# Optimization experiments

Measured on AMD Instinct MI355X. Metric: run time of the kernel, lower is better.

## Reference

```python
import math
import itertools
import jax, jax.numpy as jnp
import numpy as np

QUALITY = 95
FACTOR = (200.0 - 2.0 * QUALITY) / 100.0  # quality>=50 branch -> 0.1

# ---- constant tables (match original torch Parameters) ----
_Y = np.array([
    [16, 11, 10, 16, 24, 40, 51, 61],
    [12, 12, 14, 19, 26, 58, 60, 55],
    [14, 13, 16, 24, 40, 57, 69, 56],
    [14, 17, 22, 29, 51, 87, 80, 62],
    [18, 22, 37, 56, 68, 109, 103, 77],
    [24, 35, 55, 64, 81, 104, 113, 92],
    [49, 64, 78, 87, 103, 121, 120, 101],
    [72, 92, 95, 98, 112, 100, 103, 99]], dtype=np.float32)
Y_TABLE = jnp.asarray(_Y.T)
_C = np.full((8, 8), 99.0, dtype=np.float32)
_C[:4, :4] = np.array([[17, 18, 24, 47], [18, 21, 26, 66],
                       [24, 26, 56, 99], [47, 66, 99, 99]], dtype=np.float32).T
C_TABLE = jnp.asarray(_C)

RGB2YCBCR = jnp.asarray(np.array([
    [0.299, 0.587, 0.114],
    [-0.168736, -0.331264, 0.5],
    [0.5, -0.418688, -0.081312]], dtype=np.float32))
YCBCR2RGB = jnp.asarray(np.array([
    [1.0, 0.0, 1.402],
    [1.0, -0.344136, -0.714136],
    [1.0, 1.772, 0.0]], dtype=np.float32))

_cosmat = np.cos((2 * np.arange(8)[:, None] + 1) * np.arange(8)[None, :] * np.pi / 16).astype(np.float32)  # [x,u]
DCT_T = jnp.asarray(np.einsum('xu,yv->xyuv', _cosmat, _cosmat))   # tensor[x,y,u,v]
IDCT_T = jnp.asarray(np.einsum('ux,vy->xyuv', _cosmat, _cosmat))  # cos((2u+1)x..)cos((2v+1)y..)
_alpha = np.array([1.0 / np.sqrt(2)] + [1.0] * 7, dtype=np.float32)
ALPHA = jnp.asarray(np.outer(_alpha, _alpha))
DCT_SCALE = ALPHA * 0.25


def diff_round(x):
    s = jnp.zeros_like(x)
    for n in range(1, 10):
        s = s + ((-1.0) ** (n + 1) / n) * jnp.sin(2.0 * math.pi * n * x)
    return x - s / math.pi


def _avgpool2(x):  # [B,H,W] -> [B,H/2,W/2]
    b, h, w = x.shape
    return x.reshape(b, h // 2, 2, w // 2, 2).mean(axis=(2, 4))


def _block_split(x):  # [B,H,W] -> [B,N,8,8]
    b, h, w = x.shape
    return x.reshape(b, h // 8, 8, w // 8, 8).transpose(0, 1, 3, 2, 4).reshape(b, -1, 8, 8)


def _block_merge(p, h, w):  # [B,N,8,8] -> [B,h,w]
    b = p.shape[0]
    return p.reshape(b, h // 8, w // 8, 8, 8).transpose(0, 1, 3, 2, 4).reshape(b, h, w)


def _compress_component(comp, table):
    blocks = _block_split(comp) - 128.0
    dct = DCT_SCALE * jnp.einsum('bnxy,xyuv->bnuv', blocks, DCT_T)
    return diff_round(dct / (table * FACTOR))


def _decompress_component(q, table, h, w):
    d = q * (table * FACTOR)
    idct = 0.25 * jnp.einsum('bnxy,xyuv->bnuv', d * ALPHA, IDCT_T) + 128.0
    return _block_merge(idct, h, w)


def _diffjpeg(x):
    b, c, h, w = x.shape
    img = x * 255.0
    # RGB -> YCbCr (pixel @ RGB2YCBCR.T) + shift
    ycbcr = jnp.einsum('bchw,oc->bhwo', img, RGB2YCBCR) + jnp.array([0.0, 128.0, 128.0], dtype=x.dtype)
    y = ycbcr[..., 0]
    cb = _avgpool2(ycbcr[..., 1])
    cr = _avgpool2(ycbcr[..., 2])
    # compress
    yq = _compress_component(y, Y_TABLE)
    cbq = _compress_component(cb, C_TABLE)
    crq = _compress_component(cr, C_TABLE)
    # decompress
    y2 = _decompress_component(yq, Y_TABLE, h, w)
    cb2 = _decompress_component(cbq, C_TABLE, h // 2, w // 2)
    cr2 = _decompress_component(crq, C_TABLE, h // 2, w // 2)
    cb_up = jnp.repeat(jnp.repeat(cb2, 2, axis=1), 2, axis=2)
    cr_up = jnp.repeat(jnp.repeat(cr2, 2, axis=1), 2, axis=2)
    ycc = jnp.stack([y2, cb_up, cr_up], axis=3)  # [B,H,W,3]
    rgb = jnp.einsum('bhwc,oc->bhwo', ycc + jnp.array([0.0, -128.0, -128.0], dtype=x.dtype), YCBCR2RGB)
    rgb = rgb.transpose(0, 3, 1, 2)  # [B,3,H,W]
    rgb = jnp.clip(rgb, 0.0, 255.0)
    return rgb / 255.0


def setup_inputs() -> dict:
    key = jax.random.key(0)
    x = jax.random.uniform(key, (16, 3, 512, 512), dtype=jnp.float32)
    return {"x": x}


def reference(x):
    return _diffjpeg(x)
```

## Files before the change

kernel.cpp:

```cpp
#include <hip/hip_runtime.h>
#include <hip/hip_bf16.h>


__device__ constexpr float YTAB8[8][8] = {
    {16, 12, 14, 14, 18, 24, 49, 72},
    {11, 12, 13, 17, 22, 35, 64, 92},
    {10, 14, 16, 22, 37, 55, 78, 95},
    {16, 19, 24, 29, 56, 64, 87, 98},
    {24, 26, 40, 51, 68, 81, 103, 112},
    {40, 58, 57, 87, 109, 104, 121, 100},
    {51, 60, 69, 80, 103, 113, 120, 103},
    {61, 55, 56, 62, 77, 92, 101, 99}};

__device__ constexpr float CTAB8[8][8] = {
    {17, 18, 24, 47, 99, 99, 99, 99},
    {18, 21, 26, 66, 99, 99, 99, 99},
    {24, 26, 56, 99, 99, 99, 99, 99},
    {47, 66, 99, 99, 99, 99, 99, 99},
    {99, 99, 99, 99, 99, 99, 99, 99},
    {99, 99, 99, 99, 99, 99, 99, 99},
    {99, 99, 99, 99, 99, 99, 99, 99},
    {99, 99, 99, 99, 99, 99, 99, 99}};

#define C1f 0.9807852804032304f
#define C2f 0.9238795325112867f
#define C3f 0.8314696123025452f
#define C4f 0.7071067811865476f
#define C5f 0.5555702330196022f
#define C6f 0.3826834323650898f
#define C7f 0.1950903220161283f

__device__ __forceinline__ void dct8(float y[8]) {
    float e0=y[0]+y[7], e1=y[1]+y[6], e2=y[2]+y[5], e3=y[3]+y[4];
    float o0=y[0]-y[7], o1=y[1]-y[6], o2=y[2]-y[5], o3=y[3]-y[4];
    float t0=e0+e3, t1=e1+e2, d0=e0-e3, d1=e1-e2;
    y[0]=t0+t1; y[4]=(t0-t1)*C4f;
    y[2]=d0*C2f+d1*C6f; y[6]=d0*C6f-d1*C2f;
    y[1]=o0*C1f+o1*C3f+o2*C5f+o3*C7f;
    y[3]=o0*C3f-o1*C7f-o2*C1f-o3*C5f;
    y[5]=o0*C5f-o1*C1f+o2*C7f+o3*C3f;
    y[7]=o0*C7f-o1*C5f+o2*C3f-o3*C1f;
}

__device__ __forceinline__ void idct8(float y[8]) {
    float a=y[4]*C4f, p=y[0]+a, m=y[0]-a;
    float q=y[2]*C2f+y[6]*C6f, w=y[2]*C6f-y[6]*C2f;
    float E0=p+q, E1=m+w, E2=m-w, E3=p-q;
    float O0=y[1]*C1f+y[3]*C3f+y[5]*C5f+y[7]*C7f;
    float O1=y[1]*C3f-y[3]*C7f-y[5]*C1f-y[7]*C5f;
    float O2=y[1]*C5f-y[3]*C1f+y[5]*C7f+y[7]*C3f;
    float O3=y[1]*C7f-y[3]*C5f+y[5]*C3f-y[7]*C1f;
    y[0]=E0+O0; y[7]=E0-O0; y[1]=E1+O1; y[6]=E1-O1;
    y[2]=E2+O2; y[5]=E2-O2; y[3]=E3+O3; y[4]=E3-O3;
}

__device__ __forceinline__ void transpose8(float y[8]) {
    const int lane = threadIdx.x & 63;
#pragma unroll
    for (int s = 1; s <= 4; s <<= 1) {
        const bool upper = (lane & (s << 3)) != 0;
#pragma unroll
        for (int j = 0; j < 8; ++j) {
            if ((j & s) == 0) {
                float a = y[j], b2 = y[j | s];
                float t = upper ? a : b2;
                t = __shfl_xor(t, s << 3, 64);
                if (upper) y[j] = t; else y[j | s] = t;
            }
        }
    }
}

__device__ __forceinline__ float diff_round_f(float x) {
    float f = x - rintf(x);
    float th = 6.283185307179586f * f;
    float s1, c1v;
    __sincosf(th, &s1, &c1v);
    float twoc = 2.0f * c1v;
    float sp = 0.0f, sc = s1, acc = 0.0f;
    const float coef[9] = {1.0f, -0.5f, 1.0f/3.0f, -0.25f, 0.2f,
                           -1.0f/6.0f, 1.0f/7.0f, -0.125f, 1.0f/9.0f};
#pragma unroll
    for (int n = 0; n < 9; ++n) {
        acc += coef[n] * sc;
        float sn = twoc * sc - sp;
        sp = sc; sc = sn;
    }
    return x - acc * 0.3183098861837907f;
}

__global__ __launch_bounds__(384, 6) void diffjpeg_kernel(
        const float* __restrict__ x, float* __restrict__ out) {
    __shared__ float QS[2][128];
    __shared__ float PL[3][8][65];
    __shared__ float CL[2][8][65];

    const int tid = threadIdx.x;
    const int lane = tid & 63;
    const int r = lane >> 3;
    const int b = lane & 7;

    if (tid < 128) {
        int type = tid >> 6;
        int k = tid & 63, u = k >> 3, v = k & 7;
        float t = (type ? CTAB8[u][v] : YTAB8[u][v]) * 0.1f;
        float aa = 0.25f * ((u == 0) ? C4f : 1.0f) * ((v == 0) ? C4f : 1.0f);
        QS[type][2 * k]     = aa / t;
        QS[type][2 * k + 1] = aa * t;
    }

    const int img = blockIdx.y;
    const int sy = (blockIdx.x >> 2) * 16;
    const int sx = (blockIdx.x & 3) * 128;
    const size_t plane = (size_t)512 * 512;
    const float* src = x + (size_t)img * 3 * plane;
    float* dst = out + (size_t)img * 3 * plane;

    float y[8];
    const int w = tid >> 6;
    const int brow = w >> 1;
    const int bcol = (w & 1) * 8 + b;

    if (tid < 256) {
        const int py = sy + brow * 8 + r;
        const int px = sx + bcol * 8;
        const float* p = src + (size_t)py * 512 + px;
        float4 R0 = *(const float4*)(p);
        float4 R1 = *(const float4*)(p + 4);
        float4 G0 = *(const float4*)(p + plane);
        float4 G1 = *(const float4*)(p + plane + 4);
        float4 B0 = *(const float4*)(p + 2 * plane);
        float4 B1 = *(const float4*)(p + 2 * plane + 4);
        y[0] = 76.245f * R0.x + 149.685f * G0.x + 29.07f * B0.x - 128.0f;
        y[1] = 76.245f * R0.y + 149.685f * G0.y + 29.07f * B0.y - 128.0f;
        y[2] = 76.245f * R0.z + 149.685f * G0.z + 29.07f * B0.z - 128.0f;
        y[3] = 76.245f * R0.w + 149.685f * G0.w + 29.07f * B0.w - 128.0f;
        y[4] = 76.245f * R1.x + 149.685f * G1.x + 29.07f * B1.x - 128.0f;
        y[5] = 76.245f * R1.y + 149.685f * G1.y + 29.07f * B1.y - 128.0f;
        y[6] = 76.245f * R1.z + 149.685f * G1.z + 29.07f * B1.z - 128.0f;
        y[7] = 76.245f * R1.w + 149.685f * G1.w + 29.07f * B1.w - 128.0f;
        float rs0 = R0.x + R0.y, rs1 = R0.z + R0.w, rs2 = R1.x + R1.y, rs3 = R1.z + R1.w;
        float gs0 = G0.x + G0.y, gs1 = G0.z + G0.w, gs2 = G1.x + G1.y, gs3 = G1.z + G1.w;
        float bs0 = B0.x + B0.y, bs1 = B0.z + B0.w, bs2 = B1.x + B1.y, bs3 = B1.z + B1.w;
        rs0 += __shfl_xor(rs0, 8, 64); rs1 += __shfl_xor(rs1, 8, 64);
        rs2 += __shfl_xor(rs2, 8, 64); rs3 += __shfl_xor(rs3, 8, 64);
        gs0 += __shfl_xor(gs0, 8, 64); gs1 += __shfl_xor(gs1, 8, 64);
        gs2 += __shfl_xor(gs2, 8, 64); gs3 += __shfl_xor(gs3, 8, 64);
        bs0 += __shfl_xor(bs0, 8, 64); bs1 += __shfl_xor(bs1, 8, 64);
        bs2 += __shfl_xor(bs2, 8, 64); bs3 += __shfl_xor(bs3, 8, 64);
        if (!(r & 1)) {
            const int prow = brow * 4 + (r >> 1);
            const int pc = bcol * 4;
            PL[0][prow][pc] = rs0; PL[0][prow][pc+1] = rs1;
            PL[0][prow][pc+2] = rs2; PL[0][prow][pc+3] = rs3;
            PL[1][prow][pc] = gs0; PL[1][prow][pc+1] = gs1;
            PL[1][prow][pc+2] = gs2; PL[1][prow][pc+3] = gs3;
            PL[2][prow][pc] = bs0; PL[2][prow][pc+1] = bs1;
            PL[2][prow][pc+2] = bs2; PL[2][prow][pc+3] = bs3;
        }
    }
    __syncthreads();

    if (tid < 256) {
        dct8(y); transpose8(y); dct8(y);
        const float* qs = QS[0];
#pragma unroll
        for (int j = 0; j < 8; ++j) {
            float s1v = qs[2 * (j * 8 + r)];
            float s2v = qs[2 * (j * 8 + r) + 1];
            y[j] = diff_round_f(y[j] * s1v) * s2v;
        }
        idct8(y); transpose8(y); idct8(y);
    } else {
        const int ch = (tid >= 320);
        const float kr = ch ?  31.875f   : -10.75692f;
        const float kg = ch ? -26.69136f : -21.11808f;
        const float kb = ch ?  -5.18364f :  31.875f;
        float c[8];
#pragma unroll
        for (int j = 0; j < 8; ++j)
            c[j] = kr * PL[0][r][b * 8 + j] + kg * PL[1][r][b * 8 + j]
                 + kb * PL[2][r][b * 8 + j];
        dct8(c); transpose8(c); dct8(c);
        const float* qs = QS[1];
#pragma unroll
        for (int j = 0; j < 8; ++j) {
            float s1v = qs[2 * (j * 8 + r)];
            float s2v = qs[2 * (j * 8 + r) + 1];
            c[j] = diff_round_f(c[j] * s1v) * s2v;
        }
        idct8(c); transpose8(c); idct8(c);
#pragma unroll
        for (int j = 0; j < 8; ++j)
            CL[ch][r][b * 8 + j] = c[j];
    }
    __syncthreads();

    if (tid < 256) {
        const int prow = brow * 4 + (r >> 1);
        const int pc = bcol * 4;
        float cbv[4], crv[4];
#pragma unroll
        for (int jj = 0; jj < 4; ++jj) {
            cbv[jj] = CL[0][prow][pc + jj];
            crv[jj] = CL[1][prow][pc + jj];
        }
        float oR[8], oG[8], oB[8];
#pragma unroll
        for (int j = 0; j < 8; ++j) {
            float cb = cbv[j >> 1], cr = crv[j >> 1];
            float yv = y[j] + 128.0f;
            float R = yv + 1.402f * cr;
            float G = yv - 0.344136f * cb - 0.714136f * cr;
            float B = yv + 1.772f * cb;
            oR[j] = fminf(fmaxf(R, 0.0f), 255.0f) * (1.0f / 255.0f);
            oG[j] = fminf(fmaxf(G, 0.0f), 255.0f) * (1.0f / 255.0f);
            oB[j] = fminf(fmaxf(B, 0.0f), 255.0f) * (1.0f / 255.0f);
        }
        const int py = sy + brow * 8 + r;
        const int px = sx + bcol * 8;
        float* p = dst + (size_t)py * 512 + px;
        *(float4*)(p)                 = make_float4(oR[0], oR[1], oR[2], oR[3]);
        *(float4*)(p + 4)             = make_float4(oR[4], oR[5], oR[6], oR[7]);
        *(float4*)(p + plane)         = make_float4(oG[0], oG[1], oG[2], oG[3]);
        *(float4*)(p + plane + 4)     = make_float4(oG[4], oG[5], oG[6], oG[7]);
        *(float4*)(p + 2 * plane)     = make_float4(oB[0], oB[1], oB[2], oB[3]);
        *(float4*)(p + 2 * plane + 4) = make_float4(oB[4], oB[5], oB[6], oB[7]);
    }
}

extern "C" void kernel_launch(void* const* d_in, const int* in_sizes, int n_in,
                              void* d_out, int out_size, void* d_ws, size_t ws_size,
                              hipStream_t stream) {
    const float* x = (const float*)d_in[0];
    float* out = (float*)d_out;
    dim3 grid(128, 16);
    dim3 block(384);
    diffjpeg_kernel<<<grid, block, 0, stream>>>(x, out);
}
```

Before: 27.36 us.

## Process 32-row tiles with 256 threads, balancing luma and chroma work per wave

Each block now covers a 32x128 tile with 256 threads. Every thread handles two luma blocks and one chroma block, so the separate chroma waves that sat idle during the luma phase are gone. Chroma conversion is folded in before the pair-sum shuffle, which shrinks the shared staging to two chroma planes. diff_round now uses hardware fract/sin/cos builtins that take revolutions directly, dropping the rint and the 2*pi multiply. The trade-offs are more registers per thread and half as many blocks.

```diff
diff --git a/kernel.cpp b/kernel.cpp
--- a/kernel.cpp
+++ b/kernel.cpp
@@ -1,5 +1,4 @@
 #include <hip/hip_runtime.h>
-#include <hip/hip_bf16.h>
 
 
 __device__ constexpr float YTAB8[8][8] = {
@@ -72,12 +71,11 @@
 }
 
 __device__ __forceinline__ float diff_round_f(float x) {
-    float f = x - rintf(x);
-    float th = 6.283185307179586f * f;
-    float s1, c1v;
-    __sincosf(th, &s1, &c1v);
+    float f = __builtin_amdgcn_fractf(x);
+    float sc = __builtin_amdgcn_sinf(f);
+    float c1v = __builtin_amdgcn_cosf(f);
     float twoc = 2.0f * c1v;
-    float sp = 0.0f, sc = s1, acc = 0.0f;
+    float sp = 0.0f, acc = 0.0f;
     const float coef[9] = {1.0f, -0.5f, 1.0f/3.0f, -0.25f, 0.2f,
                            -1.0f/6.0f, 1.0f/7.0f, -0.125f, 1.0f/9.0f};
 #pragma unroll
@@ -89,16 +87,28 @@
     return x - acc * 0.3183098861837907f;
 }
 
-__global__ __launch_bounds__(384, 6) void diffjpeg_kernel(
+__device__ __forceinline__ void jpeg_block(float y[8], const float* qs, int r) {
+    dct8(y); transpose8(y); dct8(y);
+#pragma unroll
+    for (int j = 0; j < 8; ++j) {
+        float s1v = qs[2 * (j * 8 + r)];
+        float s2v = qs[2 * (j * 8 + r) + 1];
+        y[j] = diff_round_f(y[j] * s1v) * s2v;
+    }
+    idct8(y); transpose8(y); idct8(y);
+}
+
+__global__ __launch_bounds__(256, 4) void diffjpeg_kernel(
         const float* __restrict__ x, float* __restrict__ out) {
     __shared__ float QS[2][128];
-    __shared__ float PL[3][8][65];
-    __shared__ float CL[2][8][65];
+    __shared__ float PL[2][16][65];
+    __shared__ float CL[2][16][65];
 
     const int tid = threadIdx.x;
     const int lane = tid & 63;
     const int r = lane >> 3;
     const int b = lane & 7;
+    const int w = tid >> 6;
 
     if (tid < 128) {
         int type = tid >> 6;
@@ -110,95 +120,118 @@
     }
 
     const int img = blockIdx.y;
-    const int sy = (blockIdx.x >> 2) * 16;
+    const int sy = (blockIdx.x >> 2) * 32;
     const int sx = (blockIdx.x & 3) * 128;
     const size_t plane = (size_t)512 * 512;
     const float* src = x + (size_t)img * 3 * plane;
     float* dst = out + (size_t)img * 3 * plane;
 
-    float y[8];
-    const int w = tid >> 6;
-    const int brow = w >> 1;
-    const int bcol = (w & 1) * 8 + b;
-
-    if (tid < 256) {
-        const int py = sy + brow * 8 + r;
-        const int px = sx + bcol * 8;
-        const float* p = src + (size_t)py * 512 + px;
-        float4 R0 = *(const float4*)(p);
-        float4 R1 = *(const float4*)(p + 4);
-        float4 G0 = *(const float4*)(p + plane);
-        float4 G1 = *(const float4*)(p + plane + 4);
-        float4 B0 = *(const float4*)(p + 2 * plane);
-        float4 B1 = *(const float4*)(p + 2 * plane + 4);
-        y[0] = 76.245f * R0.x + 149.685f * G0.x + 29.07f * B0.x - 128.0f;
-        y[1] = 76.245f * R0.y + 149.685f * G0.y + 29.07f * B0.y - 128.0f;
-        y[2] = 76.245f * R0.z + 149.685f * G0.z + 29.07f * B0.z - 128.0f;
-        y[3] = 76.245f * R0.w + 149.685f * G0.w + 29.07f * B0.w - 128.0f;
-        y[4] = 76.245f * R1.x + 149.685f * G1.x + 29.07f * B1.x - 128.0f;
-        y[5] = 76.245f * R1.y + 149.685f * G1.y + 29.07f * B1.y - 128.0f;
-        y[6] = 76.245f * R1.z + 149.685f * G1.z + 29.07f * B1.z - 128.0f;
-        y[7] = 76.245f * R1.w + 149.685f * G1.w + 29.07f * B1.w - 128.0f;
-        float rs0 = R0.x + R0.y, rs1 = R0.z + R0.w, rs2 = R1.x + R1.y, rs3 = R1.z + R1.w;
-        float gs0 = G0.x + G0.y, gs1 = G0.z + G0.w, gs2 = G1.x + G1.y, gs3 = G1.z + G1.w;
-        float bs0 = B0.x + B0.y, bs1 = B0.z + B0.w, bs2 = B1.x + B1.y, bs3 = B1.z + B1.w;
-        rs0 += __shfl_xor(rs0, 8, 64); rs1 += __shfl_xor(rs1, 8, 64);
-        rs2 += __shfl_xor(rs2, 8, 64); rs3 += __shfl_xor(rs3, 8, 64);
-        gs0 += __shfl_xor(gs0, 8, 64); gs1 += __shfl_xor(gs1, 8, 64);
-        gs2 += __shfl_xor(gs2, 8, 64); gs3 += __shfl_xor(gs3, 8, 64);
-        bs0 += __shfl_xor(bs0, 8, 64); bs1 += __shfl_xor(bs1, 8, 64);
-        bs2 += __shfl_xor(bs2, 8, 64); bs3 += __shfl_xor(bs3, 8, 64);
+    const int browA = w >> 1;
+    const int bcol  = (w & 1) * 8 + b;
+    const int px  = sx + bcol * 8;
+    const int pyA = sy + browA * 8 + r;
+    const int pyB = pyA + 16;
+
+    float yA[8], yB[8];
+    {
+        const float* pa = src + (size_t)pyA * 512 + px;
+        const float* pb = src + (size_t)pyB * 512 + px;
+        float4 RA0 = *(const float4*)(pa);
+        float4 RA1 = *(const float4*)(pa + 4);
+        float4 GA0 = *(const float4*)(pa + plane);
+        float4 GA1 = *(const float4*)(pa + plane + 4);
+        float4 BA0 = *(const float4*)(pa + 2 * plane);
+        float4 BA1 = *(const float4*)(pa + 2 * plane + 4);
+        float4 RB0 = *(const float4*)(pb);
+        float4 RB1 = *(const float4*)(pb + 4);
+        float4 GB0 = *(const float4*)(pb + plane);
+        float4 GB1 = *(const float4*)(pb + plane + 4);
+        float4 BB0 = *(const float4*)(pb + 2 * plane);
+        float4 BB1 = *(const float4*)(pb + 2 * plane + 4);
+
+        yA[0] = 76.245f*RA0.x + 149.685f*GA0.x + 29.07f*BA0.x - 128.0f;
+        yA[1] = 76.245f*RA0.y + 149.685f*GA0.y + 29.07f*BA0.y - 128.0f;
+        yA[2] = 76.245f*RA0.z + 149.685f*GA0.z + 29.07f*BA0.z - 128.0f;
+        yA[3] = 76.245f*RA0.w + 149.685f*GA0.w + 29.07f*BA0.w - 128.0f;
+        yA[4] = 76.245f*RA1.x + 149.685f*GA1.x + 29.07f*BA1.x - 128.0f;
+        yA[5] = 76.245f*RA1.y + 149.685f*GA1.y + 29.07f*BA1.y - 128.0f;
+        yA[6] = 76.245f*RA1.z + 149.685f*GA1.z + 29.07f*BA1.z - 128.0f;
+        yA[7] = 76.245f*RA1.w + 149.685f*GA1.w + 29.07f*BA1.w - 128.0f;
+        yB[0] = 76.245f*RB0.x + 149.685f*GB0.x + 29.07f*BB0.x - 128.0f;
+        yB[1] = 76.245f*RB0.y + 149.685f*GB0.y + 29.07f*BB0.y - 128.0f;
+        yB[2] = 76.245f*RB0.z + 149.685f*GB0.z + 29.07f*BB0.z - 128.0f;
+        yB[3] = 76.245f*RB0.w + 149.685f*GB0.w + 29.07f*BB0.w - 128.0f;
+        yB[4] = 76.245f*RB1.x + 149.685f*GB1.x + 29.07f*BB1.x - 128.0f;
+        yB[5] = 76.245f*RB1.y + 149.685f*GB1.y + 29.07f*BB1.y - 128.0f;
+        yB[6] = 76.245f*RB1.z + 149.685f*GB1.z + 29.07f*BB1.z - 128.0f;
+        yB[7] = 76.245f*RB1.w + 149.685f*GB1.w + 29.07f*BB1.w - 128.0f;
+
+        const float kbr = -10.75692f, kbg = -21.11808f, kbb = 31.875f;
+        const float krr =  31.875f,   krg = -26.69136f, krb = -5.18364f;
+        float cbA[4], crA[4], cbB[4], crB[4];
+        {
+            float rh0=RA0.x+RA0.y, rh1=RA0.z+RA0.w, rh2=RA1.x+RA1.y, rh3=RA1.z+RA1.w;
+            float gh0=GA0.x+GA0.y, gh1=GA0.z+GA0.w, gh2=GA1.x+GA1.y, gh3=GA1.z+GA1.w;
+            float bh0=BA0.x+BA0.y, bh1=BA0.z+BA0.w, bh2=BA1.x+BA1.y, bh3=BA1.z+BA1.w;
+            cbA[0]=kbr*rh0+kbg*gh0+kbb*bh0; cbA[1]=kbr*rh1+kbg*gh1+kbb*bh1;
+            cbA[2]=kbr*rh2+kbg*gh2+kbb*bh2; cbA[3]=kbr*rh3+kbg*gh3+kbb*bh3;
+            crA[0]=krr*rh0+krg*gh0+krb*bh0; crA[1]=krr*rh1+krg*gh1+krb*bh1;
+            crA[2]=krr*rh2+krg*gh2+krb*bh2; crA[3]=krr*rh3+krg*gh3+krb*bh3;
+        }
+        {
+            float rh0=RB0.x+RB0.y, rh1=RB0.z+RB0.w, rh2=RB1.x+RB1.y, rh3=RB1.z+RB1.w;
+            float gh0=GB0.x+GB0.y, gh1=GB0.z+GB0.w, gh2=GB1.x+GB1.y, gh3=GB1.z+GB1.w;
+            float bh0=BB0.x+BB0.y, bh1=BB0.z+BB0.w, bh2=BB1.x+BB1.y, bh3=BB1.z+BB1.w;
+            cbB[0]=kbr*rh0+kbg*gh0+kbb*bh0; cbB[1]=kbr*rh1+kbg*gh1+kbb*bh1;
+            cbB[2]=kbr*rh2+kbg*gh2+kbb*bh2; cbB[3]=kbr*rh3+kbg*gh3+kbb*bh3;
+            crB[0]=krr*rh0+krg*gh0+krb*bh0; crB[1]=krr*rh1+krg*gh1+krb*bh1;
+            crB[2]=krr*rh2+krg*gh2+krb*bh2; crB[3]=krr*rh3+krg*gh3+krb*bh3;
+        }
+#pragma unroll
+        for (int k = 0; k < 4; ++k) {
+            cbA[k] += __shfl_xor(cbA[k], 8, 64);
+            crA[k] += __shfl_xor(crA[k], 8, 64);
+            cbB[k] += __shfl_xor(cbB[k], 8, 64);
+            crB[k] += __shfl_xor(crB[k], 8, 64);
+        }
         if (!(r & 1)) {
-            const int prow = brow * 4 + (r >> 1);
+            const int prowA = browA * 4 + (r >> 1);
+            const int prowB = prowA + 8;
             const int pc = bcol * 4;
-            PL[0][prow][pc] = rs0; PL[0][prow][pc+1] = rs1;
-            PL[0][prow][pc+2] = rs2; PL[0][prow][pc+3] = rs3;
-            PL[1][prow][pc] = gs0; PL[1][prow][pc+1] = gs1;
-            PL[1][prow][pc+2] = gs2; PL[1][prow][pc+3] = gs3;
-            PL[2][prow][pc] = bs0; PL[2][prow][pc+1] = bs1;
-            PL[2][prow][pc+2] = bs2; PL[2][prow][pc+3] = bs3;
+#pragma unroll
+            for (int k = 0; k < 4; ++k) {
+                PL[0][prowA][pc + k] = cbA[k];
+                PL[1][prowA][pc + k] = crA[k];
+                PL[0][prowB][pc + k] = cbB[k];
+                PL[1][prowB][pc + k] = crB[k];
+            }
         }
     }
     __syncthreads();
 
-    if (tid < 256) {
-        dct8(y); transpose8(y); dct8(y);
-        const float* qs = QS[0];
-#pragma unroll
-        for (int j = 0; j < 8; ++j) {
-            float s1v = qs[2 * (j * 8 + r)];
-            float s2v = qs[2 * (j * 8 + r) + 1];
-            y[j] = diff_round_f(y[j] * s1v) * s2v;
-        }
-        idct8(y); transpose8(y); idct8(y);
-    } else {
-        const int ch = (tid >= 320);
-        const float kr = ch ?  31.875f   : -10.75692f;
-        const float kg = ch ? -26.69136f : -21.11808f;
-        const float kb = ch ?  -5.18364f :  31.875f;
+    jpeg_block(yA, QS[0], r);
+    jpeg_block(yB, QS[0], r);
+
+    {
+        const int chw  = w >> 1;
+        const int cblk = (w & 1) * 8 + b;
+        const int crow = (cblk >> 3) * 8 + r;
+        const int ccol = (cblk & 7) * 8;
         float c[8];
 #pragma unroll
-        for (int j = 0; j < 8; ++j)
-            c[j] = kr * PL[0][r][b * 8 + j] + kg * PL[1][r][b * 8 + j]
-                 + kb * PL[2][r][b * 8 + j];
-        dct8(c); transpose8(c); dct8(c);
-        const float* qs = QS[1];
-#pragma unroll
-        for (int j = 0; j < 8; ++j) {
-            float s1v = qs[2 * (j * 8 + r)];
-            float s2v = qs[2 * (j * 8 + r) + 1];
-            c[j] = diff_round_f(c[j] * s1v) * s2v;
-        }
-        idct8(c); transpose8(c); idct8(c);
-#pragma unroll
-        for (int j = 0; j < 8; ++j)
-            CL[ch][r][b * 8 + j] = c[j];
+        for (int j = 0; j < 8; ++j) c[j] = PL[chw][crow][ccol + j];
+        jpeg_block(c, QS[1], r);
+#pragma unroll
+        for (int j = 0; j < 8; ++j) CL[chw][crow][ccol + j] = c[j];
     }
     __syncthreads();
 
-    if (tid < 256) {
-        const int prow = brow * 4 + (r >> 1);
-        const int pc = bcol * 4;
+    const int pc = bcol * 4;
+#pragma unroll
+    for (int blkI = 0; blkI < 2; ++blkI) {
+        const float* yv8 = blkI ? yB : yA;
+        const int prow = browA * 4 + (r >> 1) + blkI * 8;
+        const int py   = blkI ? pyB : pyA;
         float cbv[4], crv[4];
 #pragma unroll
         for (int jj = 0; jj < 4; ++jj) {
@@ -209,7 +242,7 @@
 #pragma unroll
         for (int j = 0; j < 8; ++j) {
             float cb = cbv[j >> 1], cr = crv[j >> 1];
-            float yv = y[j] + 128.0f;
+            float yv = yv8[j] + 128.0f;
             float R = yv + 1.402f * cr;
             float G = yv - 0.344136f * cb - 0.714136f * cr;
             float B = yv + 1.772f * cb;
@@ -217,8 +250,6 @@
             oG[j] = fminf(fmaxf(G, 0.0f), 255.0f) * (1.0f / 255.0f);
             oB[j] = fminf(fmaxf(B, 0.0f), 255.0f) * (1.0f / 255.0f);
         }
-        const int py = sy + brow * 8 + r;
-        const int px = sx + bcol * 8;
         float* p = dst + (size_t)py * 512 + px;
         *(float4*)(p)                 = make_float4(oR[0], oR[1], oR[2], oR[3]);
         *(float4*)(p + 4)             = make_float4(oR[4], oR[5], oR[6], oR[7]);
@@ -234,7 +265,7 @@
                               hipStream_t stream) {
     const float* x = (const float*)d_in[0];
     float* out = (float*)d_out;
-    dim3 grid(128, 16);
-    dim3 block(384);
+    dim3 grid(64, 16);
+    dim3 block(256);
     diffjpeg_kernel<<<grid, block, 0, stream>>>(x, out);
 }
```

Result: faster. 25.72 us (-6.0%).

## Use single-wave blocks with per-block chroma and hardware sin/cos rounding

Applied to the files above, without the earlier changes.

Shrinks each block to one 64-lane wave covering a 16x32 tile. Every wave now handles its own luma blocks plus the chroma blocks, instead of 6-wave blocks where two waves sit idle during luma work. Chroma Cb/Cr are computed before the shuffle reduction, so only two planes go to LDS instead of three. diff_round now uses the hardware fract, sin and cos builtins, which take revolutions directly, in place of rintf plus __sincosf. The risks are redundant chroma work (half the chroma lanes compute duplicates), many more small blocks, and a different sin precision.

```diff
diff --git a/kernel.cpp b/kernel.cpp
--- a/kernel.cpp
+++ b/kernel.cpp
@@ -1,5 +1,4 @@
 #include <hip/hip_runtime.h>
-#include <hip/hip_bf16.h>
 
 
 __device__ constexpr float YTAB8[8][8] = {
@@ -72,12 +71,11 @@
 }
 
 __device__ __forceinline__ float diff_round_f(float x) {
-    float f = x - rintf(x);
-    float th = 6.283185307179586f * f;
-    float s1, c1v;
-    __sincosf(th, &s1, &c1v);
+    float f = __builtin_amdgcn_fractf(x);
+    float sc = __builtin_amdgcn_sinf(f);
+    float c1v = __builtin_amdgcn_cosf(f);
     float twoc = 2.0f * c1v;
-    float sp = 0.0f, sc = s1, acc = 0.0f;
+    float sp = 0.0f, acc = 0.0f;
     const float coef[9] = {1.0f, -0.5f, 1.0f/3.0f, -0.25f, 0.2f,
                            -1.0f/6.0f, 1.0f/7.0f, -0.125f, 1.0f/9.0f};
 #pragma unroll
@@ -89,41 +87,49 @@
     return x - acc * 0.3183098861837907f;
 }
 
-__global__ __launch_bounds__(384, 6) void diffjpeg_kernel(
+__device__ __forceinline__ void jpeg_block(float y[8], const float* qs, int r) {
+    dct8(y); transpose8(y); dct8(y);
+#pragma unroll
+    for (int j = 0; j < 8; ++j) {
+        float s1v = qs[2 * (j * 8 + r)];
+        float s2v = qs[2 * (j * 8 + r) + 1];
+        y[j] = diff_round_f(y[j] * s1v) * s2v;
+    }
+    idct8(y); transpose8(y); idct8(y);
+}
+
+__global__ __launch_bounds__(64, 4) void diffjpeg_kernel(
         const float* __restrict__ x, float* __restrict__ out) {
     __shared__ float QS[2][128];
-    __shared__ float PL[3][8][65];
-    __shared__ float CL[2][8][65];
+    __shared__ float PL[2][8][17];
+    __shared__ float CL[2][8][17];
 
     const int tid = threadIdx.x;
-    const int lane = tid & 63;
-    const int r = lane >> 3;
-    const int b = lane & 7;
-
-    if (tid < 128) {
-        int type = tid >> 6;
-        int k = tid & 63, u = k >> 3, v = k & 7;
-        float t = (type ? CTAB8[u][v] : YTAB8[u][v]) * 0.1f;
+    const int r = tid >> 3;
+    const int b = tid & 7;
+
+    {
+        const int u = r, v = b;
+        float ty = YTAB8[u][v] * 0.1f;
+        float tc = CTAB8[u][v] * 0.1f;
         float aa = 0.25f * ((u == 0) ? C4f : 1.0f) * ((v == 0) ? C4f : 1.0f);
-        QS[type][2 * k]     = aa / t;
-        QS[type][2 * k + 1] = aa * t;
+        QS[0][2 * tid] = aa / ty; QS[0][2 * tid + 1] = aa * ty;
+        QS[1][2 * tid] = aa / tc; QS[1][2 * tid + 1] = aa * tc;
     }
 
     const int img = blockIdx.y;
-    const int sy = (blockIdx.x >> 2) * 16;
-    const int sx = (blockIdx.x & 3) * 128;
+    const int sy = (blockIdx.x >> 4) * 16;
+    const int sx = (blockIdx.x & 15) * 32;
     const size_t plane = (size_t)512 * 512;
     const float* src = x + (size_t)img * 3 * plane;
     float* dst = out + (size_t)img * 3 * plane;
 
+    const int br = b >> 2, bc = b & 3;
+    const int py = sy + br * 8 + r;
+    const int px = sx + bc * 8;
+
     float y[8];
-    const int w = tid >> 6;
-    const int brow = w >> 1;
-    const int bcol = (w & 1) * 8 + b;
-
-    if (tid < 256) {
-        const int py = sy + brow * 8 + r;
-        const int px = sx + bcol * 8;
+    {
         const float* p = src + (size_t)py * 512 + px;
         float4 R0 = *(const float4*)(p);
         float4 R1 = *(const float4*)(p + 4);
@@ -131,74 +137,60 @@
         float4 G1 = *(const float4*)(p + plane + 4);
         float4 B0 = *(const float4*)(p + 2 * plane);
         float4 B1 = *(const float4*)(p + 2 * plane + 4);
-        y[0] = 76.245f * R0.x + 149.685f * G0.x + 29.07f * B0.x - 128.0f;
-        y[1] = 76.245f * R0.y + 149.685f * G0.y + 29.07f * B0.y - 128.0f;
-        y[2] = 76.245f * R0.z + 149.685f * G0.z + 29.07f * B0.z - 128.0f;
-        y[3] = 76.245f * R0.w + 149.685f * G0.w + 29.07f * B0.w - 128.0f;
-        y[4] = 76.245f * R1.x + 149.685f * G1.x + 29.07f * B1.x - 128.0f;
-        y[5] = 76.245f * R1.y + 149.685f * G1.y + 29.07f * B1.y - 128.0f;
-        y[6] = 76.245f * R1.z + 149.685f * G1.z + 29.07f * B1.z - 128.0f;
-        y[7] = 76.245f * R1.w + 149.685f * G1.w + 29.07f * B1.w - 128.0f;
-        float rs0 = R0.x + R0.y, rs1 = R0.z + R0.w, rs2 = R1.x + R1.y, rs3 = R1.z + R1.w;
-        float gs0 = G0.x + G0.y, gs1 = G0.z + G0.w, gs2 = G1.x + G1.y, gs3 = G1.z + G1.w;
-        float bs0 = B0.x + B0.y, bs1 = B0.z + B0.w, bs2 = B1.x + B1.y, bs3 = B1.z + B1.w;
-        rs0 += __shfl_xor(rs0, 8, 64); rs1 += __shfl_xor(rs1, 8, 64);
-        rs2 += __shfl_xor(rs2, 8, 64); rs3 += __shfl_xor(rs3, 8, 64);
-        gs0 += __shfl_xor(gs0, 8, 64); gs1 += __shfl_xor(gs1, 8, 64);
-        gs2 += __shfl_xor(gs2, 8, 64); gs3 += __shfl_xor(gs3, 8, 64);
-        bs0 += __shfl_xor(bs0, 8, 64); bs1 += __shfl_xor(bs1, 8, 64);
-        bs2 += __shfl_xor(bs2, 8, 64); bs3 += __shfl_xor(bs3, 8, 64);
+        y[0] = 76.245f*R0.x + 149.685f*G0.x + 29.07f*B0.x - 128.0f;
+        y[1] = 76.245f*R0.y + 149.685f*G0.y + 29.07f*B0.y - 128.0f;
+        y[2] = 76.245f*R0.z + 149.685f*G0.z + 29.07f*B0.z - 128.0f;
+        y[3] = 76.245f*R0.w + 149.685f*G0.w + 29.07f*B0.w - 128.0f;
+        y[4] = 76.245f*R1.x + 149.685f*G1.x + 29.07f*B1.x - 128.0f;
+        y[5] = 76.245f*R1.y + 149.685f*G1.y + 29.07f*B1.y - 128.0f;
+        y[6] = 76.245f*R1.z + 149.685f*G1.z + 29.07f*B1.z - 128.0f;
+        y[7] = 76.245f*R1.w + 149.685f*G1.w + 29.07f*B1.w - 128.0f;
+        float rh0=R0.x+R0.y, rh1=R0.z+R0.w, rh2=R1.x+R1.y, rh3=R1.z+R1.w;
+        float gh0=G0.x+G0.y, gh1=G0.z+G0.w, gh2=G1.x+G1.y, gh3=G1.z+G1.w;
+        float bh0=B0.x+B0.y, bh1=B0.z+B0.w, bh2=B1.x+B1.y, bh3=B1.z+B1.w;
+        const float kbr = -10.75692f, kbg = -21.11808f, kbb = 31.875f;
+        const float krr =  31.875f,   krg = -26.69136f, krb = -5.18364f;
+        float cb[4], cr[4];
+        cb[0]=kbr*rh0+kbg*gh0+kbb*bh0; cb[1]=kbr*rh1+kbg*gh1+kbb*bh1;
+        cb[2]=kbr*rh2+kbg*gh2+kbb*bh2; cb[3]=kbr*rh3+kbg*gh3+kbb*bh3;
+        cr[0]=krr*rh0+krg*gh0+krb*bh0; cr[1]=krr*rh1+krg*gh1+krb*bh1;
+        cr[2]=krr*rh2+krg*gh2+krb*bh2; cr[3]=krr*rh3+krg*gh3+krb*bh3;
+#pragma unroll
+        for (int k = 0; k < 4; ++k) {
+            cb[k] += __shfl_xor(cb[k], 8, 64);
+            cr[k] += __shfl_xor(cr[k], 8, 64);
+        }
         if (!(r & 1)) {
-            const int prow = brow * 4 + (r >> 1);
-            const int pc = bcol * 4;
-            PL[0][prow][pc] = rs0; PL[0][prow][pc+1] = rs1;
-            PL[0][prow][pc+2] = rs2; PL[0][prow][pc+3] = rs3;
-            PL[1][prow][pc] = gs0; PL[1][prow][pc+1] = gs1;
-            PL[1][prow][pc+2] = gs2; PL[1][prow][pc+3] = gs3;
-            PL[2][prow][pc] = bs0; PL[2][prow][pc+1] = bs1;
-            PL[2][prow][pc+2] = bs2; PL[2][prow][pc+3] = bs3;
+            const int prow = br * 4 + (r >> 1);
+            const int pc = bc * 4;
+#pragma unroll
+            for (int k = 0; k < 4; ++k) {
+                PL[0][prow][pc + k] = cb[k];
+                PL[1][prow][pc + k] = cr[k];
+            }
         }
     }
     __syncthreads();
 
-    if (tid < 256) {
-        dct8(y); transpose8(y); dct8(y);
-        const float* qs = QS[0];
-#pragma unroll
-        for (int j = 0; j < 8; ++j) {
-            float s1v = qs[2 * (j * 8 + r)];
-            float s2v = qs[2 * (j * 8 + r) + 1];
-            y[j] = diff_round_f(y[j] * s1v) * s2v;
-        }
-        idct8(y); transpose8(y); idct8(y);
-    } else {
-        const int ch = (tid >= 320);
-        const float kr = ch ?  31.875f   : -10.75692f;
-        const float kg = ch ? -26.69136f : -21.11808f;
-        const float kb = ch ?  -5.18364f :  31.875f;
+    jpeg_block(y, QS[0], r);
+
+    {
+        const int ch = (b >> 1) & 1;
+        const int cblk = b & 1;
         float c[8];
 #pragma unroll
-        for (int j = 0; j < 8; ++j)
-            c[j] = kr * PL[0][r][b * 8 + j] + kg * PL[1][r][b * 8 + j]
-                 + kb * PL[2][r][b * 8 + j];
-        dct8(c); transpose8(c); dct8(c);
-        const float* qs = QS[1];
-#pragma unroll
-        for (int j = 0; j < 8; ++j) {
-            float s1v = qs[2 * (j * 8 + r)];
-            float s2v = qs[2 * (j * 8 + r) + 1];
-            c[j] = diff_round_f(c[j] * s1v) * s2v;
-        }
-        idct8(c); transpose8(c); idct8(c);
-#pragma unroll
-        for (int j = 0; j < 8; ++j)
-            CL[ch][r][b * 8 + j] = c[j];
+        for (int j = 0; j < 8; ++j) c[j] = PL[ch][r][cblk * 8 + j];
+        jpeg_block(c, QS[1], r);
+        if (b < 4) {
+#pragma unroll
+            for (int j = 0; j < 8; ++j) CL[ch][r][cblk * 8 + j] = c[j];
+        }
     }
     __syncthreads();
 
-    if (tid < 256) {
-        const int prow = brow * 4 + (r >> 1);
-        const int pc = bcol * 4;
+    {
+        const int prow = br * 4 + (r >> 1);
+        const int pc = bc * 4;
         float cbv[4], crv[4];
 #pragma unroll
         for (int jj = 0; jj < 4; ++jj) {
@@ -217,8 +209,6 @@
             oG[j] = fminf(fmaxf(G, 0.0f), 255.0f) * (1.0f / 255.0f);
             oB[j] = fminf(fmaxf(B, 0.0f), 255.0f) * (1.0f / 255.0f);
         }
-        const int py = sy + brow * 8 + r;
-        const int px = sx + bcol * 8;
         float* p = dst + (size_t)py * 512 + px;
         *(float4*)(p)                 = make_float4(oR[0], oR[1], oR[2], oR[3]);
         *(float4*)(p + 4)             = make_float4(oR[4], oR[5], oR[6], oR[7]);
@@ -234,7 +224,7 @@
                               hipStream_t stream) {
     const float* x = (const float*)d_in[0];
     float* out = (float*)d_out;
-    dim3 grid(128, 16);
-    dim3 block(384);
+    dim3 grid(512, 16);
+    dim3 block(64);
     diffjpeg_kernel<<<grid, block, 0, stream>>>(x, out);
 }
```

Result: faster. 24.88 us (-9.1%).
